# Performance work log

Measured on AMD Instinct MI355X. Metric: run time of the kernel, lower is better.

## Reference

```python
import jax, jax.numpy as jnp
import numpy as np
from jax import lax

# Shared Conv2d [1,1] + BN + ReLU is represented as a per-point affine (BN folded
# into conv weight/bias at eval) followed by ReLU, matching inference-mode math.

B, N1, N2, K = 8, 8192, 2048, 8
C1, C2 = 64, 128
MLP0, MLP1, MLP2 = 128, 128, 128  # mlp=[128,128], mlp2=[128]


def setup_inputs() -> dict:
    key = jax.random.key(0)
    ks = jax.random.split(key, 10)
    sc = lambda fan_in: 1.0 / np.sqrt(fan_in)
    return {
        "xyz1": jax.random.normal(ks[0], (B, N1, 3), jnp.float32),
        "xyz2": jax.random.normal(ks[1], (B, N2, 3), jnp.float32),
        "feat1": jax.random.normal(ks[2], (B, N1, C1), jnp.float32),
        "feat2": jax.random.normal(ks[3], (B, N2, C2), jnp.float32),
        "W0": jax.random.normal(ks[4], (C2 + 3, MLP0), jnp.float32) * sc(C2 + 3),
        "b0": jnp.zeros((MLP0,), jnp.float32),
        "W1": jax.random.normal(ks[5], (MLP0, MLP1), jnp.float32) * sc(MLP0),
        "b1": jnp.zeros((MLP1,), jnp.float32),
        "W2": jax.random.normal(ks[6], (MLP1 + C1, MLP2), jnp.float32) * sc(MLP1 + C1),
        "b2": jnp.zeros((MLP2,), jnp.float32),
    }


def _knn_idx(xyz1, xyz2, k):
    # squared distances (B, N1, N2); top-k nearest in xyz2 for each xyz1 point
    d2 = jnp.sum((xyz1[:, :, None, :] - xyz2[:, None, :, :]) ** 2, axis=-1)
    _, idx = lax.top_k(-d2, k)  # (B, N1, K)
    return idx


def _gather(src, idx):
    # src: (B, N2, C), idx: (B, N1, K) -> (B, N1, K, C)
    return jax.vmap(lambda s, i: s[i])(src, idx)


def reference(xyz1, xyz2, feat1, feat2, W0, b0, W1, b1, W2, b2):
    idx = _knn_idx(xyz1, xyz2, K)
    xyz2_g = _gather(xyz2, idx)            # (B, N1, K, 3)
    feat2_g = _gather(feat2, idx)          # (B, N1, K, C2)
    xyz_diff = xyz2_g - xyz1[:, :, None, :]
    net = jnp.concatenate([feat2_g, xyz_diff], axis=-1)  # (B, N1, K, C2+3)
    net = jax.nn.relu(net @ W0 + b0)
    net = jax.nn.relu(net @ W1 + b1)       # (B, N1, K, MLP1)
    pooled = jnp.max(net, axis=2)          # max pooling over neighbors
    cat = jnp.concatenate([pooled, feat1], axis=-1)      # (B, N1, MLP1+C1)
    out = jax.nn.relu(cat @ W2 + b2)       # (B, N1, MLP2)
    return out
```

## Files before the change

kernel.cpp:

```cpp
#include <hip/hip_runtime.h>
#include <hip/hip_bf16.h>

constexpr int B_  = 8;
constexpr int N1_ = 8192;
constexpr int N2_ = 2048;
constexpr int K_  = 8;

typedef short bf16x8 __attribute__((ext_vector_type(8)));
typedef float f32x4  __attribute__((ext_vector_type(4)));

__device__ __forceinline__ short f2b(float x) {
    __hip_bfloat16 h = __float2bfloat16(x);
    return *reinterpret_cast<short*>(&h);
}

__global__ __launch_bounds__(256) void prep_feat2(const float* __restrict__ feat2,
                                                  short* __restrict__ feat2b) {
    const int i = blockIdx.x * 256 + threadIdx.x;
    const float4 v = ((const float4*)feat2)[i];
    uint2 o;
    o.x = (unsigned short)f2b(v.x) | ((unsigned)(unsigned short)f2b(v.y) << 16);
    o.y = (unsigned short)f2b(v.z) | ((unsigned)(unsigned short)f2b(v.w) << 16);
    ((uint2*)feat2b)[i] = o;
}

__global__ __launch_bounds__(256) void prep_weights(
    const float* __restrict__ W0, const float* __restrict__ W1,
    const float* __restrict__ W2, const float* __restrict__ xyz2,
    short* __restrict__ W0T, short* __restrict__ W1T, short* __restrict__ W2T,
    float4* __restrict__ xpack) {
    int i = blockIdx.x * 256 + threadIdx.x;
    if (i < 128 * 160) {
        const int n = i / 160, k = i % 160;
        W0T[i] = (k < 131) ? f2b(W0[k * 128 + n]) : (short)0;
        return;
    }
    i -= 128 * 160;
    if (i < 128 * 128) {
        const int n = i >> 7, k = i & 127;
        W1T[i] = f2b(W1[k * 128 + n]);
        return;
    }
    i -= 128 * 128;
    if (i < 128 * 192) {
        const int n = i / 192, k = i % 192;
        W2T[i] = f2b(W2[k * 128 + n]);
        return;
    }
    i -= 128 * 192;
    xpack[i] = make_float4(xyz2[i * 3 + 0], xyz2[i * 3 + 1], xyz2[i * 3 + 2], 0.f);
}

__global__ __launch_bounds__(256) void knn_seg(const float* __restrict__ xyz1,
                                               const float4* __restrict__ xpack,
                                               int* __restrict__ idx) {
    __shared__ float sD[64][33];
    __shared__ int   sI[64][33];

    const int b = blockIdx.y;
    const int lane = threadIdx.x & 63;
    const int s = threadIdx.x >> 6;
    const int n = blockIdx.x * 64 + lane;

    const float* q = xyz1 + ((size_t)b * N1_ + n) * 3;
    const float qx = q[0], qy = q[1], qz = q[2];
    const float4* P = xpack + (size_t)b * N2_ + s * 512;

    float bd[K_];
    int   bi[K_];
#pragma unroll
    for (int t = 0; t < K_; ++t) { bd[t] = 3.0e38f; bi[t] = 0; }

    for (int j0 = 0; j0 < 512; j0 += 8) {
        float d2[8];
#pragma unroll
        for (int u = 0; u < 8; ++u) {
#pragma clang fp contract(off)
            const float4 p = P[j0 + u];
            const float dx = qx - p.x;
            const float dy = qy - p.y;
            const float dz = qz - p.z;
            const float dx2 = dx * dx;
            const float dy2 = dy * dy;
            const float dz2 = dz * dz;
            d2[u] = (dx2 + dy2) + dz2;
        }
        float mn = d2[0];
#pragma unroll
        for (int u = 1; u < 8; ++u) mn = fminf(mn, d2[u]);
        if (mn < bd[K_ - 1]) {
#pragma unroll
            for (int u = 0; u < 8; ++u) {
                if (d2[u] < bd[K_ - 1]) {
                    bd[K_ - 1] = d2[u]; bi[K_ - 1] = s * 512 + j0 + u;
#pragma unroll
                    for (int t = K_ - 1; t >= 1; --t) {
                        if (bd[t] < bd[t - 1]) {
                            float td = bd[t]; bd[t] = bd[t - 1]; bd[t - 1] = td;
                            int   ti = bi[t]; bi[t] = bi[t - 1]; bi[t - 1] = ti;
                        }
                    }
                }
            }
        }
    }

#pragma unroll
    for (int t = 0; t < K_; ++t) { sD[lane][s * 8 + t] = bd[t]; sI[lane][s * 8 + t] = bi[t]; }
    __syncthreads();

    if (threadIdx.x < 64) {
        const int qq = threadIdx.x;
        int h[4] = {0, 0, 0, 0};
        const int base = (b * N1_ + n) * K_;
#pragma unroll
        for (int t = 0; t < K_; ++t) {
            float best = 3.1e38f;
            int   bidx = 0, bs = 0;
#pragma unroll
            for (int ss = 0; ss < 4; ++ss) {
                if (h[ss] < 8) {
                    const float d = sD[qq][ss * 8 + h[ss]];
                    if (d < best) { best = d; bidx = sI[qq][ss * 8 + h[ss]]; bs = ss; }
                }
            }
            h[bs]++;
            idx[base + t] = bidx;
        }
    }
}

__global__ __launch_bounds__(256) void fused_mfma(
    const float* __restrict__ xyz1, const float* __restrict__ xyz2,
    const float* __restrict__ feat1,
    const float* __restrict__ b0, const float* __restrict__ b1,
    const float* __restrict__ b2,
    const short* __restrict__ feat2b, const short* __restrict__ W0T,
    const short* __restrict__ W1T, const short* __restrict__ W2T,
    const int* __restrict__ idx, float* __restrict__ out) {
    __shared__ __align__(16) short sA[128 * 168];
    __shared__ __align__(16) short sCat[16 * 200];

    const int b = blockIdx.y;
    const int n0 = blockIdx.x * 16;
    const int tid = threadIdx.x;

    {
        const int row = tid >> 1, half = tid & 1;
        const int p = row >> 3, kk = row & 7;
        const int n = n0 + p;
        const int j = idx[((size_t)b * N1_ + n) * K_ + kk];
        const uint4* src = (const uint4*)(feat2b + ((size_t)(b * N2_ + j)) * 128 + half * 64);
        uint4* dst = (uint4*)(sA + row * 168 + half * 64);
#pragma unroll
        for (int t = 0; t < 8; ++t) dst[t] = src[t];
        uint4* pad = (uint4*)(sA + row * 168 + 128 + half * 16);
        if (half == 0) {
            const float dx = xyz2[((size_t)b * N2_ + j) * 3 + 0] - xyz1[((size_t)b * N1_ + n) * 3 + 0];
            const float dy = xyz2[((size_t)b * N2_ + j) * 3 + 1] - xyz1[((size_t)b * N1_ + n) * 3 + 1];
            const float dz = xyz2[((size_t)b * N2_ + j) * 3 + 2] - xyz1[((size_t)b * N1_ + n) * 3 + 2];
            uint4 v;
            v.x = (unsigned short)f2b(dx) | ((unsigned)(unsigned short)f2b(dy) << 16);
            v.y = (unsigned short)f2b(dz);
            v.z = 0; v.w = 0;
            pad[0] = v;
            pad[1] = make_uint4(0, 0, 0, 0);
        } else {
            pad[0] = make_uint4(0, 0, 0, 0);
            pad[1] = make_uint4(0, 0, 0, 0);
        }
    }
    {
#pragma unroll
        for (int u = 0; u < 4; ++u) {
            const int e = tid * 4 + u;
            const int p = e >> 6, c = e & 63;
            sCat[p * 200 + 128 + c] = f2b(feat1[((size_t)b * N1_ + n0 + p) * 64 + c]);
        }
    }
    __syncthreads();

    const int wave = tid >> 6, lane = tid & 63;
    const int q = lane >> 4, l15 = lane & 15;
    const int mBase = (wave & 1) * 64, nBase = (wave >> 1) * 64;

    const f32x4 zero4 = {0.f, 0.f, 0.f, 0.f};

    f32x4 acc[4][4];
#pragma unroll
    for (int mt = 0; mt < 4; ++mt)
#pragma unroll
        for (int nt = 0; nt < 4; ++nt) acc[mt][nt] = zero4;

    for (int ks = 0; ks < 5; ++ks) {
        bf16x8 af[4], bf[4];
#pragma unroll
        for (int mt = 0; mt < 4; ++mt)
            af[mt] = *(const bf16x8*)(sA + (mBase + mt * 16 + l15) * 168 + ks * 32 + q * 8);
#pragma unroll
        for (int nt = 0; nt < 4; ++nt)
            bf[nt] = *(const bf16x8*)(W0T + (nBase + nt * 16 + l15) * 160 + ks * 32 + q * 8);
#pragma unroll
        for (int mt = 0; mt < 4; ++mt)
#pragma unroll
            for (int nt = 0; nt < 4; ++nt)
                acc[mt][nt] = __builtin_amdgcn_mfma_f32_16x16x32_bf16(af[mt], bf[nt], acc[mt][nt], 0, 0, 0);
    }

    float b0v[4];
#pragma unroll
    for (int nt = 0; nt < 4; ++nt) b0v[nt] = b0[nBase + nt * 16 + l15];
    __syncthreads();
#pragma unroll
    for (int mt = 0; mt < 4; ++mt)
#pragma unroll
        for (int nt = 0; nt < 4; ++nt)
#pragma unroll
            for (int r = 0; r < 4; ++r) {
                const int row = mBase + mt * 16 + q * 4 + r;
                const int col = nBase + nt * 16 + l15;
                sA[row * 136 + col] = f2b(fmaxf(acc[mt][nt][r] + b0v[nt], 0.f));
            }
    __syncthreads();

    f32x4 acc2[4][4];
#pragma unroll
    for (int mt = 0; mt < 4; ++mt)
#pragma unroll
        for (int nt = 0; nt < 4; ++nt) acc2[mt][nt] = zero4;

    for (int ks = 0; ks < 4; ++ks) {
        bf16x8 af[4], bf[4];
#pragma unroll
        for (int mt = 0; mt < 4; ++mt)
            af[mt] = *(const bf16x8*)(sA + (mBase + mt * 16 + l15) * 136 + ks * 32 + q * 8);
#pragma unroll
        for (int nt = 0; nt < 4; ++nt)
            bf[nt] = *(const bf16x8*)(W1T + (nBase + nt * 16 + l15) * 128 + ks * 32 + q * 8);
#pragma unroll
        for (int mt = 0; mt < 4; ++mt)
#pragma unroll
            for (int nt = 0; nt < 4; ++nt)
                acc2[mt][nt] = __builtin_amdgcn_mfma_f32_16x16x32_bf16(af[mt], bf[nt], acc2[mt][nt], 0, 0, 0);
    }

    float b1v[4];
#pragma unroll
    for (int nt = 0; nt < 4; ++nt) b1v[nt] = b1[nBase + nt * 16 + l15];
#pragma unroll
    for (int mt = 0; mt < 4; ++mt)
#pragma unroll
        for (int nt = 0; nt < 4; ++nt) {
            float vm = fmaxf(acc2[mt][nt][0] + b1v[nt], 0.f);
#pragma unroll
            for (int r = 1; r < 4; ++r) vm = fmaxf(vm, acc2[mt][nt][r] + b1v[nt]);
            const float other = __shfl_xor(vm, 16);
            const float pool = fmaxf(vm, other);
            if ((q & 1) == 0) {
                const int pp = (mBase >> 3) + mt * 2 + (q >> 1);
                sCat[pp * 200 + nBase + nt * 16 + l15] = f2b(pool);
            }
        }
    __syncthreads();

    f32x4 acc3[2];
    acc3[0] = zero4; acc3[1] = zero4;
    const int nB2 = wave * 32;
    for (int ks = 0; ks < 6; ++ks) {
        const bf16x8 a2 = *(const bf16x8*)(sCat + l15 * 200 + ks * 32 + q * 8);
#pragma unroll
        for (int nt = 0; nt < 2; ++nt) {
            const bf16x8 b2f = *(const bf16x8*)(W2T + (nB2 + nt * 16 + l15) * 192 + ks * 32 + q * 8);
            acc3[nt] = __builtin_amdgcn_mfma_f32_16x16x32_bf16(a2, b2f, acc3[nt], 0, 0, 0);
        }
    }
    float b2v[2];
#pragma unroll
    for (int nt = 0; nt < 2; ++nt) b2v[nt] = b2[nB2 + nt * 16 + l15];
#pragma unroll
    for (int nt = 0; nt < 2; ++nt)
#pragma unroll
        for (int r = 0; r < 4; ++r) {
            const int p = q * 4 + r;
            const int col = nB2 + nt * 16 + l15;
            out[((size_t)(b * N1_ + n0 + p)) * 128 + col] = fmaxf(acc3[nt][r] + b2v[nt], 0.f);
        }
}

extern "C" void kernel_launch(void* const* d_in, const int* in_sizes, int n_in,
                              void* d_out, int out_size, void* d_ws, size_t ws_size,
                              hipStream_t stream) {
    const float* xyz1  = (const float*)d_in[0];
    const float* xyz2  = (const float*)d_in[1];
    const float* feat1 = (const float*)d_in[2];
    const float* feat2 = (const float*)d_in[3];
    const float* W0    = (const float*)d_in[4];
    const float* b0    = (const float*)d_in[5];
    const float* W1    = (const float*)d_in[6];
    const float* b1    = (const float*)d_in[7];
    const float* W2    = (const float*)d_in[8];
    const float* b2    = (const float*)d_in[9];
    float* out = (float*)d_out;

    char* ws = (char*)d_ws;
    int*    idx    = (int*)(ws + 0);
    short*  feat2b = (short*)(ws + 2097152);
    short*  W0T    = (short*)(ws + 6291456);
    short*  W1T    = (short*)(ws + 6332416);
    short*  W2T    = (short*)(ws + 6365184);
    float4* xpack  = (float4*)(ws + 6414336);

    prep_feat2<<<2048, 256, 0, stream>>>(feat2, feat2b);
    prep_weights<<<304, 256, 0, stream>>>(W0, W1, W2, xyz2, W0T, W1T, W2T, xpack);
    knn_seg<<<dim3(N1_ / 64, B_), 256, 0, stream>>>(xyz1, xpack, idx);
    fused_mfma<<<dim3(N1_ / 16, B_), 256, 0, stream>>>(xyz1, xyz2, feat1, b0, b1, b2,
                                                       feat2b, W0T, W1T, W2T, idx, out);
}
```

Measured before the change: 330.2 us.

## Use branchless candidate-list KNN and gather MFMA A operands directly from global

Result: slower. 359.1 us (+8.7%).

```diff
diff --git a/kernel.cpp b/kernel.cpp
--- a/kernel.cpp
+++ b/kernel.cpp
@@ -51,25 +51,29 @@
     xpack[i] = make_float4(xyz2[i * 3 + 0], xyz2[i * 3 + 1], xyz2[i * 3 + 2], 0.f);
 }
 
-__global__ __launch_bounds__(256) void knn_seg(const float* __restrict__ xyz1,
-                                               const float4* __restrict__ xpack,
-                                               int* __restrict__ idx) {
-    __shared__ float sD[64][33];
-    __shared__ int   sI[64][33];
+constexpr int LCAP = 76;
+
+__global__ __launch_bounds__(256) void knn_list(const float* __restrict__ xyz1,
+                                                const float4* __restrict__ xpack,
+                                                int* __restrict__ idx) {
+    __shared__ __align__(16) unsigned short sMem[256 * 78];
+    float* sD = (float*)sMem;
+    int*   sI = (int*)sMem + 64 * 33;
 
     const int b = blockIdx.y;
     const int lane = threadIdx.x & 63;
     const int s = threadIdx.x >> 6;
+    const int tid = threadIdx.x;
     const int n = blockIdx.x * 64 + lane;
 
     const float* q = xyz1 + ((size_t)b * N1_ + n) * 3;
     const float qx = q[0], qy = q[1], qz = q[2];
     const float4* P = xpack + (size_t)b * N2_ + s * 512;
 
-    float bd[K_];
-    int   bi[K_];
-#pragma unroll
-    for (int t = 0; t < K_; ++t) { bd[t] = 3.0e38f; bi[t] = 0; }
+    unsigned bd[K_];
+#pragma unroll
+    for (int t = 0; t < K_; ++t) bd[t] = __float_as_uint(3.0e38f);
+    int cnt = 0;
 
     for (int j0 = 0; j0 < 512; j0 += 8) {
         float d2[8];
@@ -85,19 +89,76 @@
             const float dz2 = dz * dz;
             d2[u] = (dx2 + dy2) + dz2;
         }
-        float mn = d2[0];
-#pragma unroll
-        for (int u = 1; u < 8; ++u) mn = fminf(mn, d2[u]);
-        if (mn < bd[K_ - 1]) {
-#pragma unroll
-            for (int u = 0; u < 8; ++u) {
-                if (d2[u] < bd[K_ - 1]) {
-                    bd[K_ - 1] = d2[u]; bi[K_ - 1] = s * 512 + j0 + u;
-#pragma unroll
-                    for (int t = K_ - 1; t >= 1; --t) {
-                        if (bd[t] < bd[t - 1]) {
-                            float td = bd[t]; bd[t] = bd[t - 1]; bd[t - 1] = td;
-                            int   ti = bi[t]; bi[t] = bi[t - 1]; bi[t - 1] = ti;
+#pragma unroll
+        for (int u = 0; u < 8; ++u) {
+            const unsigned xu = __float_as_uint(d2[u]);
+            const bool acc = xu < bd[K_ - 1];
+            const int slot = acc ? (cnt < LCAP ? cnt : LCAP) : LCAP + 1;
+            sMem[tid * 78 + slot] = (unsigned short)(j0 + u);
+            cnt += acc ? 1 : 0;
+            bd[K_ - 1] = bd[K_ - 1] < xu ? bd[K_ - 1] : xu;
+#pragma unroll
+            for (int t = K_ - 1; t >= 1; --t) {
+                const unsigned lo = bd[t - 1] < bd[t] ? bd[t - 1] : bd[t];
+                const unsigned hi = bd[t - 1] < bd[t] ? bd[t] : bd[t - 1];
+                bd[t - 1] = lo; bd[t] = hi;
+            }
+        }
+    }
+
+    float rd[K_];
+    int   ri[K_];
+#pragma unroll
+    for (int t = 0; t < K_; ++t) { rd[t] = 3.0e38f; ri[t] = 0; }
+    const int m = cnt < LCAP ? cnt : LCAP;
+    for (int t = 0;; ++t) {
+        const bool act = t < m;
+        if (!__any(act)) break;
+        if (act) {
+#pragma clang fp contract(off)
+            const int jl = sMem[tid * 78 + t];
+            const float4 p = P[jl];
+            const float dx = qx - p.x;
+            const float dy = qy - p.y;
+            const float dz = qz - p.z;
+            const float dx2 = dx * dx;
+            const float dy2 = dy * dy;
+            const float dz2 = dz * dz;
+            const float d2 = (dx2 + dy2) + dz2;
+            if (d2 < rd[K_ - 1]) {
+                rd[K_ - 1] = d2; ri[K_ - 1] = s * 512 + jl;
+#pragma unroll
+                for (int t2 = K_ - 1; t2 >= 1; --t2) {
+                    if (rd[t2] < rd[t2 - 1]) {
+                        float td = rd[t2]; rd[t2] = rd[t2 - 1]; rd[t2 - 1] = td;
+                        int   ti = ri[t2]; ri[t2] = ri[t2 - 1]; ri[t2 - 1] = ti;
+                    }
+                }
+            }
+        }
+    }
+
+    if (__any(cnt > LCAP)) {
+        if (cnt > LCAP) {
+#pragma unroll
+            for (int t = 0; t < K_; ++t) { rd[t] = 3.0e38f; ri[t] = 0; }
+            for (int j = 0; j < 512; ++j) {
+#pragma clang fp contract(off)
+                const float4 p = P[j];
+                const float dx = qx - p.x;
+                const float dy = qy - p.y;
+                const float dz = qz - p.z;
+                const float dx2 = dx * dx;
+                const float dy2 = dy * dy;
+                const float dz2 = dz * dz;
+                const float d2 = (dx2 + dy2) + dz2;
+                if (d2 < rd[K_ - 1]) {
+                    rd[K_ - 1] = d2; ri[K_ - 1] = s * 512 + j;
+#pragma unroll
+                    for (int t2 = K_ - 1; t2 >= 1; --t2) {
+                        if (rd[t2] < rd[t2 - 1]) {
+                            float td = rd[t2]; rd[t2] = rd[t2 - 1]; rd[t2 - 1] = td;
+                            int   ti = ri[t2]; ri[t2] = ri[t2 - 1]; ri[t2 - 1] = ti;
                         }
                     }
                 }
@@ -105,12 +166,16 @@
         }
     }
 
-#pragma unroll
-    for (int t = 0; t < K_; ++t) { sD[lane][s * 8 + t] = bd[t]; sI[lane][s * 8 + t] = bi[t]; }
     __syncthreads();
-
-    if (threadIdx.x < 64) {
-        const int qq = threadIdx.x;
+#pragma unroll
+    for (int t = 0; t < K_; ++t) {
+        sD[lane * 33 + s * 8 + t] = rd[t];
+        sI[lane * 33 + s * 8 + t] = ri[t];
+    }
+    __syncthreads();
+
+    if (tid < 64) {
+        const int qq = tid;
         int h[4] = {0, 0, 0, 0};
         const int base = (b * N1_ + n) * K_;
 #pragma unroll
@@ -120,8 +185,8 @@
 #pragma unroll
             for (int ss = 0; ss < 4; ++ss) {
                 if (h[ss] < 8) {
-                    const float d = sD[qq][ss * 8 + h[ss]];
-                    if (d < best) { best = d; bidx = sI[qq][ss * 8 + h[ss]]; bs = ss; }
+                    const float d = sD[qq * 33 + ss * 8 + h[ss]];
+                    if (d < best) { best = d; bidx = sI[qq * 33 + ss * 8 + h[ss]]; bs = ss; }
                 }
             }
             h[bs]++;
@@ -138,51 +203,47 @@
     const short* __restrict__ feat2b, const short* __restrict__ W0T,
     const short* __restrict__ W1T, const short* __restrict__ W2T,
     const int* __restrict__ idx, float* __restrict__ out) {
-    __shared__ __align__(16) short sA[128 * 168];
+    __shared__ __align__(16) short sA1[128 * 136];
     __shared__ __align__(16) short sCat[16 * 200];
 
     const int b = blockIdx.y;
     const int n0 = blockIdx.x * 16;
     const int tid = threadIdx.x;
-
-    {
-        const int row = tid >> 1, half = tid & 1;
+    const int wave = tid >> 6, lane = tid & 63;
+    const int q = lane >> 4, l15 = lane & 15;
+    const int mBase = (wave & 1) * 64, nBase = (wave >> 1) * 64;
+
+#pragma unroll
+    for (int u = 0; u < 4; ++u) {
+        const int e = tid * 4 + u;
+        const int p = e >> 6, c = e & 63;
+        sCat[p * 200 + 128 + c] = f2b(feat1[((size_t)b * N1_ + n0 + p) * 64 + c]);
+    }
+
+    int jrow[4];
+#pragma unroll
+    for (int mt = 0; mt < 4; ++mt) {
+        const int row = mBase + mt * 16 + l15;
         const int p = row >> 3, kk = row & 7;
-        const int n = n0 + p;
-        const int j = idx[((size_t)b * N1_ + n) * K_ + kk];
-        const uint4* src = (const uint4*)(feat2b + ((size_t)(b * N2_ + j)) * 128 + half * 64);
-        uint4* dst = (uint4*)(sA + row * 168 + half * 64);
-#pragma unroll
-        for (int t = 0; t < 8; ++t) dst[t] = src[t];
-        uint4* pad = (uint4*)(sA + row * 168 + 128 + half * 16);
-        if (half == 0) {
+        jrow[mt] = idx[((size_t)b * N1_ + (n0 + p)) * K_ + kk];
+    }
+
+    bf16x8 a4[4];
+#pragma unroll
+    for (int mt = 0; mt < 4; ++mt) {
+        bf16x8 v = {0, 0, 0, 0, 0, 0, 0, 0};
+        if (q == 0) {
+            const int row = mBase + mt * 16 + l15;
+            const int p = row >> 3;
+            const int n = n0 + p;
+            const int j = jrow[mt];
             const float dx = xyz2[((size_t)b * N2_ + j) * 3 + 0] - xyz1[((size_t)b * N1_ + n) * 3 + 0];
             const float dy = xyz2[((size_t)b * N2_ + j) * 3 + 1] - xyz1[((size_t)b * N1_ + n) * 3 + 1];
             const float dz = xyz2[((size_t)b * N2_ + j) * 3 + 2] - xyz1[((size_t)b * N1_ + n) * 3 + 2];
-            uint4 v;
-            v.x = (unsigned short)f2b(dx) | ((unsigned)(unsigned short)f2b(dy) << 16);
-            v.y = (unsigned short)f2b(dz);
-            v.z = 0; v.w = 0;
-            pad[0] = v;
-            pad[1] = make_uint4(0, 0, 0, 0);
-        } else {
-            pad[0] = make_uint4(0, 0, 0, 0);
-            pad[1] = make_uint4(0, 0, 0, 0);
-        }
-    }
-    {
-#pragma unroll
-        for (int u = 0; u < 4; ++u) {
-            const int e = tid * 4 + u;
-            const int p = e >> 6, c = e & 63;
-            sCat[p * 200 + 128 + c] = f2b(feat1[((size_t)b * N1_ + n0 + p) * 64 + c]);
-        }
-    }
-    __syncthreads();
-
-    const int wave = tid >> 6, lane = tid & 63;
-    const int q = lane >> 4, l15 = lane & 15;
-    const int mBase = (wave & 1) * 64, nBase = (wave >> 1) * 64;
+            v[0] = f2b(dx); v[1] = f2b(dy); v[2] = f2b(dz);
+        }
+        a4[mt] = v;
+    }
 
     const f32x4 zero4 = {0.f, 0.f, 0.f, 0.f};
 
@@ -192,11 +253,12 @@
 #pragma unroll
         for (int nt = 0; nt < 4; ++nt) acc[mt][nt] = zero4;
 
-    for (int ks = 0; ks < 5; ++ks) {
+#pragma unroll
+    for (int ks = 0; ks < 4; ++ks) {
         bf16x8 af[4], bf[4];
 #pragma unroll
         for (int mt = 0; mt < 4; ++mt)
-            af[mt] = *(const bf16x8*)(sA + (mBase + mt * 16 + l15) * 168 + ks * 32 + q * 8);
+            af[mt] = *(const bf16x8*)(feat2b + ((size_t)b * N2_ + jrow[mt]) * 128 + ks * 32 + q * 8);
 #pragma unroll
         for (int nt = 0; nt < 4; ++nt)
             bf[nt] = *(const bf16x8*)(W0T + (nBase + nt * 16 + l15) * 160 + ks * 32 + q * 8);
@@ -206,11 +268,21 @@
             for (int nt = 0; nt < 4; ++nt)
                 acc[mt][nt] = __builtin_amdgcn_mfma_f32_16x16x32_bf16(af[mt], bf[nt], acc[mt][nt], 0, 0, 0);
     }
+    {
+        bf16x8 bf[4];
+#pragma unroll
+        for (int nt = 0; nt < 4; ++nt)
+            bf[nt] = *(const bf16x8*)(W0T + (nBase + nt * 16 + l15) * 160 + 128 + q * 8);
+#pragma unroll
+        for (int mt = 0; mt < 4; ++mt)
+#pragma unroll
+            for (int nt = 0; nt < 4; ++nt)
+                acc[mt][nt] = __builtin_amdgcn_mfma_f32_16x16x32_bf16(a4[mt], bf[nt], acc[mt][nt], 0, 0, 0);
+    }
 
     float b0v[4];
 #pragma unroll
     for (int nt = 0; nt < 4; ++nt) b0v[nt] = b0[nBase + nt * 16 + l15];
-    __syncthreads();
 #pragma unroll
     for (int mt = 0; mt < 4; ++mt)
 #pragma unroll
@@ -219,7 +291,7 @@
             for (int r = 0; r < 4; ++r) {
                 const int row = mBase + mt * 16 + q * 4 + r;
                 const int col = nBase + nt * 16 + l15;
-                sA[row * 136 + col] = f2b(fmaxf(acc[mt][nt][r] + b0v[nt], 0.f));
+                sA1[row * 136 + col] = f2b(fmaxf(acc[mt][nt][r] + b0v[nt], 0.0f));
             }
     __syncthreads();
 
@@ -229,11 +301,12 @@
 #pragma unroll
         for (int nt = 0; nt < 4; ++nt) acc2[mt][nt] = zero4;
 
+#pragma unroll
     for (int ks = 0; ks < 4; ++ks) {
         bf16x8 af[4], bf[4];
 #pragma unroll
         for (int mt = 0; mt < 4; ++mt)
-            af[mt] = *(const bf16x8*)(sA + (mBase + mt * 16 + l15) * 136 + ks * 32 + q * 8);
+            af[mt] = *(const bf16x8*)(sA1 + (mBase + mt * 16 + l15) * 136 + ks * 32 + q * 8);
 #pragma unroll
         for (int nt = 0; nt < 4; ++nt)
             bf[nt] = *(const bf16x8*)(W1T + (nBase + nt * 16 + l15) * 128 + ks * 32 + q * 8);
@@ -251,7 +324,7 @@
     for (int mt = 0; mt < 4; ++mt)
 #pragma unroll
         for (int nt = 0; nt < 4; ++nt) {
-            float vm = fmaxf(acc2[mt][nt][0] + b1v[nt], 0.f);
+            float vm = fmaxf(acc2[mt][nt][0] + b1v[nt], 0.0f);
 #pragma unroll
             for (int r = 1; r < 4; ++r) vm = fmaxf(vm, acc2[mt][nt][r] + b1v[nt]);
             const float other = __shfl_xor(vm, 16);
@@ -266,6 +339,7 @@
     f32x4 acc3[2];
     acc3[0] = zero4; acc3[1] = zero4;
     const int nB2 = wave * 32;
+#pragma unroll
     for (int ks = 0; ks < 6; ++ks) {
         const bf16x8 a2 = *(const bf16x8*)(sCat + l15 * 200 + ks * 32 + q * 8);
 #pragma unroll
@@ -283,7 +357,7 @@
         for (int r = 0; r < 4; ++r) {
             const int p = q * 4 + r;
             const int col = nB2 + nt * 16 + l15;
-            out[((size_t)(b * N1_ + n0 + p)) * 128 + col] = fmaxf(acc3[nt][r] + b2v[nt], 0.f);
+            out[((size_t)(b * N1_ + n0 + p)) * 128 + col] = fmaxf(acc3[nt][r] + b2v[nt], 0.0f);
         }
 }
 
@@ -312,7 +386,7 @@
 
     prep_feat2<<<2048, 256, 0, stream>>>(feat2, feat2b);
     prep_weights<<<304, 256, 0, stream>>>(W0, W1, W2, xyz2, W0T, W1T, W2T, xpack);
-    knn_seg<<<dim3(N1_ / 64, B_), 256, 0, stream>>>(xyz1, xpack, idx);
+    knn_list<<<dim3(N1_ / 64, B_), 256, 0, stream>>>(xyz1, xpack, idx);
     fused_mfma<<<dim3(N1_ / 16, B_), 256, 0, stream>>>(xyz1, xyz2, feat1, b0, b1, b2,
                                                        feat2b, W0T, W1T, W2T, idx, out);
 }
```
